# Kernel tuning notes

Measured on AMD Instinct MI355X. Metric: run time of the kernel, lower is better.

Reference implementation:

```python
import jax, jax.numpy as jnp
import numpy as np

BS, T, G, C = 64, 128, 36, 256
H = 256          # gaze LSTM hidden
P = 256          # spatial projected size
PT = 256         # temporal projected size
Q = 16           # queue size
NC = 10          # num classes
NEG = -1e9


def setup_inputs() -> dict:
    key = jax.random.key(0)
    ks = jax.random.split(key, 40)
    s = 0.02
    D = C + H
    inp = {
        'cnn_feat_seq': jax.random.normal(ks[0], (BS, T, G, C), jnp.float32),
        'gaze_seq': jax.random.normal(ks[1], (BS, T, 3), jnp.float32),
        # init-hidden / init-cell MLPs (Linear(3,H), Tanh, Linear(H,H), Tanh)
        'init_h_w1': jax.random.normal(ks[2], (H, 3)) * s, 'init_h_b1': jnp.zeros((H,)),
        'init_h_w2': jax.random.normal(ks[3], (H, H)) * s, 'init_h_b2': jnp.zeros((H,)),
        'init_c_w1': jax.random.normal(ks[4], (H, 3)) * s, 'init_c_b1': jnp.zeros((H,)),
        'init_c_w2': jax.random.normal(ks[5], (H, H)) * s, 'init_c_b2': jnp.zeros((H,)),
        # LSTM (input 3, hidden H), torch gate order i,f,g,o
        'lstm_wih': jax.random.normal(ks[6], (4 * H, 3)) * s, 'lstm_whh': jax.random.normal(ks[7], (4 * H, H)) * s,
        'lstm_bih': jnp.zeros((4 * H,)), 'lstm_bhh': jnp.zeros((4 * H,)),
        # spatial attention
        'sa_wl': jax.random.normal(ks[8], (P, H)) * s, 'sa_bl': jnp.zeros((P,)),
        'sa_wc': jax.random.normal(ks[9], (P, C)) * s, 'sa_bc': jnp.zeros((P,)),
        'sa_wz': jax.random.normal(ks[10], (P,)) * s,
        # temporal attention
        'ta_wl': jax.random.normal(ks[11], (PT, H)) * s, 'ta_bl': jnp.zeros((PT,)),
        'ta_wv': jax.random.normal(ks[12], (PT, C)) * s, 'ta_bv': jnp.zeros((PT,)),
        'ta_wz': jax.random.normal(ks[13], (PT,)) * s,
        # MLP classifier: Linear(D,D) -> Linear(D,D) -> Linear(D,NC), no nonlinearity
        'mlp_w1': jax.random.normal(ks[14], (D, D)) * s, 'mlp_b1': jnp.zeros((D,)),
        'mlp_w2': jax.random.normal(ks[15], (D, D)) * s, 'mlp_b2': jnp.zeros((D,)),
        'mlp_w3': jax.random.normal(ks[16], (NC, D)) * s, 'mlp_b3': jnp.zeros((NC,)),
    }
    return inp


def _forward(cnn_feat_seq, gaze_seq,
             init_h_w1, init_h_b1, init_h_w2, init_h_b2,
             init_c_w1, init_c_b1, init_c_w2, init_c_b2,
             lstm_wih, lstm_whh, lstm_bih, lstm_bhh,
             sa_wl, sa_bl, sa_wc, sa_bc, sa_wz,
             ta_wl, ta_bl, ta_wv, ta_bv, ta_wz,
             mlp_w1, mlp_b1, mlp_w2, mlp_b2, mlp_w3, mlp_b3):
    bs, num_frame = gaze_seq.shape[0], gaze_seq.shape[1]
    mean_gaze = jnp.mean(gaze_seq, axis=1)  # (bs, 3)
    # init MLP ends with Tanh, and forward applies F.tanh again
    h0 = jnp.tanh(jnp.tanh(jnp.tanh(mean_gaze @ init_h_w1.T + init_h_b1) @ init_h_w2.T + init_h_b2))
    c0 = jnp.tanh(jnp.tanh(jnp.tanh(mean_gaze @ init_c_w1.T + init_c_b1) @ init_c_w2.T + init_c_b2))
    buf_s0 = jnp.zeros((Q, bs, C), cnn_feat_seq.dtype)
    buf_h0 = jnp.zeros((Q, bs, H), cnn_feat_seq.dtype)
    qidx = jnp.arange(Q)

    def step(carry, xs):
        h, c, buf_s, buf_h, i = carry
        feat, gaze = xs  # (bs,G,C), (bs,3)
        # --- spatial additive attention over grids ---
        Hp = h @ sa_wl.T + sa_bl                                  # (bs,P)
        Vp = jnp.einsum('bgc,pc->bgp', feat, sa_wc) + sa_bc       # (bs,G,P)
        zs = jnp.tanh(Hp[:, None, :] + Vp) @ sa_wz                # (bs,G)
        sw = jax.nn.softmax(zs, axis=1)
        spat = jnp.einsum('bgc,bg->bc', feat, sw)                 # (bs,C)
        # --- rolling queues (newest last) ---
        buf_s = jnp.concatenate([buf_s[1:], spat[None]], axis=0)
        buf_h = jnp.concatenate([buf_h[1:], h[None]], axis=0)
        count = jnp.minimum(i + 1, Q)
        mask = qidx >= (Q - count)                                # (Q,) valid slots
        # --- temporal additive attention over queue ---
        Hq = jnp.einsum('qbh,ph->qbp', buf_h, ta_wl) + ta_bl
        Vq = jnp.einsum('qbc,pc->qbp', buf_s, ta_wv) + ta_bv
        zt = jnp.tanh(Hq + Vq) @ ta_wz                            # (Q,bs)
        zt = jnp.where(mask[:, None], zt, NEG)
        tw = jax.nn.softmax(zt, axis=0)
        temp = jnp.einsum('qbc,qb->bc', buf_s, tw)                # (bs,C)
        # --- one LSTM step on gaze ---
        gates = gaze @ lstm_wih.T + lstm_bih + h @ lstm_whh.T + lstm_bhh
        gi, gf, gg, go = jnp.split(gates, 4, axis=-1)
        c = jax.nn.sigmoid(gf) * c + jax.nn.sigmoid(gi) * jnp.tanh(gg)
        h = jax.nn.sigmoid(go) * jnp.tanh(c)
        # --- classifier on concat(temporal_feat, lstm_hidden) ---
        fc = jnp.concatenate([temp, h], axis=1)                   # (bs, C+H)
        pred = ((fc @ mlp_w1.T + mlp_b1) @ mlp_w2.T + mlp_b2) @ mlp_w3.T + mlp_b3
        return (h, c, buf_s, buf_h, i + 1), pred

    feats_t = jnp.swapaxes(cnn_feat_seq, 0, 1)  # (T,bs,G,C)
    gaze_t = jnp.swapaxes(gaze_seq, 0, 1)       # (T,bs,3)
    _, preds = jax.lax.scan(step, (h0, c0, buf_s0, buf_h0, jnp.int32(0)), (feats_t, gaze_t))
    # torch cats (1,bs,NC) pieces along dim=1 -> (1, T*bs, NC)
    return preds.reshape(1, num_frame * bs, NC)


def reference(cnn_feat_seq, gaze_seq,
              init_h_w1, init_h_b1, init_h_w2, init_h_b2,
              init_c_w1, init_c_b1, init_c_w2, init_c_b2,
              lstm_wih, lstm_whh, lstm_bih, lstm_bhh,
              sa_wl, sa_bl, sa_wc, sa_bc, sa_wz,
              ta_wl, ta_bl, ta_wv, ta_bv, ta_wz,
              mlp_w1, mlp_b1, mlp_w2, mlp_b2, mlp_w3, mlp_b3):
    return _forward(cnn_feat_seq, gaze_seq,
                    init_h_w1, init_h_b1, init_h_w2, init_h_b2,
                    init_c_w1, init_c_b1, init_c_w2, init_c_b2,
                    lstm_wih, lstm_whh, lstm_bih, lstm_bhh,
                    sa_wl, sa_bl, sa_wc, sa_bc, sa_wz,
                    ta_wl, ta_bl, ta_wv, ta_bv, ta_wz,
                    mlp_w1, mlp_b1, mlp_w2, mlp_b2, mlp_w3, mlp_b3)
```

## Files before the change

### kernel.cpp

```cpp
#include <hip/hip_runtime.h>
#include <cstdint>
#include <cstddef>

#define BSZ 64
#define TT  128
#define GG  36
#define CC  256
#define HH  256
#define QQ  16
#define NCLS 10
#define NROW 8192
#define SP_ROWS 16

using short8  = __attribute__((ext_vector_type(8))) short;
using f32x4   = __attribute__((ext_vector_type(4))) float;
using half2_t = __attribute__((ext_vector_type(2))) _Float16;
typedef unsigned int u32;
typedef unsigned short u16;

#define OFF_WI    0u
#define OFF_WF    131072u
#define OFF_WG    262144u
#define OFF_WO    393216u
#define OFF_SAWL  524288u
#define OFF_TAWL  655360u
#define OFF_TAWV  786432u
#define OFF_SAWC  917504u
#define OFF_W32   1048576u
#define OFF_WC    1069056u
#define OFF_BC    1089536u
#define OFF_H0F16 1089792u
#define OFF_C0    1122560u
#define OFF_HSEQ  1188096u
#define OFF_HSEQB 9642240u
#define OFF_HPSA  13869312u
#define OFF_HQ    22257920u
#define OFF_SPAT  30646528u
#define OFF_SPATB 39035136u
#define OFF_ZSC   43229440u
#define WS_NEEDED 43262208u

__device__ __forceinline__ float rcp_fast(float x){
#if __has_builtin(__builtin_amdgcn_rcpf)
  return __builtin_amdgcn_rcpf(x);
#else
  return 1.f/x;
#endif
}
__device__ __forceinline__ float fast_sig(float x){ return rcp_fast(1.f+__expf(-x)); }
__device__ __forceinline__ float fast_tanh(float x){ float e=__expf(2.f*x); return 1.f-2.f*rcp_fast(e+1.f); }
__device__ __forceinline__ u16 f2bf(float f){
  u32 u = __builtin_bit_cast(u32, f);
  u += 0x7fffu + ((u>>16)&1u);
  return (u16)(u>>16);
}
__device__ __forceinline__ float bf2f(u16 b){
  u32 u = ((u32)b)<<16; return __builtin_bit_cast(float, u);
}
__device__ __forceinline__ u32 cvtpk_bf16(float a, float b){
  u32 p;
  asm("v_cvt_pk_bf16_f32 %0, %1, %2" : "=v"(p) : "v"(a), "v"(b));
  return p;
}
__device__ __forceinline__ u32 packf16(float a, float b){
  half2_t h; h.x = (_Float16)a; h.y = (_Float16)b;
  return __builtin_bit_cast(u32, h);
}
__device__ __forceinline__ float dot2(u32 w, u32 h, float acc){
#if __has_builtin(__builtin_amdgcn_fdot2)
  return __builtin_amdgcn_fdot2(__builtin_bit_cast(half2_t, w),
                                __builtin_bit_cast(half2_t, h), acc, false);
#else
  half2_t a = __builtin_bit_cast(half2_t, w), b = __builtin_bit_cast(half2_t, h);
  return acc + (float)a.x*(float)b.x + (float)a.y*(float)b.y;
#endif
}
__device__ __forceinline__ f32x4 mfma16(short8 a, short8 b, f32x4 c){
  return __builtin_amdgcn_mfma_f32_16x16x32_bf16(a, b, c, 0, 0, 0);
}

__global__ void __launch_bounds__(256) k_prep1(const float* __restrict__ whh,
    const float* __restrict__ sawl, const float* __restrict__ tawl,
    const float* __restrict__ tawv, const float* __restrict__ sawc,
    const float* __restrict__ w3, const float* __restrict__ w2, char* ws){
  int blk = blockIdx.x, tid = threadIdx.x;
  if (blk < 512){
    u32* wq = (u32*)ws;
    for (int rr = 0; rr < 2; ++rr){
      int row = blk*2 + rr;
      float v  = whh[row*256 + tid];
      float vn = __shfl_down(v, 1);
      if ((tid & 1) == 0){
        int typ = row >> 8;
        int j   = row & 255;
        wq[typ*32768 + (tid>>1)*256 + j] = packf16(v, vn);
      }
    }
  } else if (blk < 544){
    int rel = blk - 512;
    int mat = rel >> 3;
    const float* src; u16* dst;
    if (mat==0){ src=sawl; dst=(u16*)(ws+OFF_SAWL); }
    else if (mat==1){ src=tawl; dst=(u16*)(ws+OFF_TAWL); }
    else if (mat==2){ src=tawv; dst=(u16*)(ws+OFF_TAWV); }
    else { src=sawc; dst=(u16*)(ws+OFF_SAWC); }
    int base = (rel & 7)*8192 + tid;
    if (mat < 3){
      for (int i = 0; i < 32; ++i){ int e = base + i*256; dst[e] = f2bf(src[e]); }
    } else {
      for (int i = 0; i < 32; ++i){
        int e = base + i*256;
        int col = e >> 8, kk = e & 255;
        dst[col*256 + (kk ^ ((col&7)<<3))] = f2bf(src[e]);
      }
    }
  } else {
    int idx = (blk-544)*256 + tid;
    int o = idx >> 9, k2 = idx & 511;
    float acc = 0.f;
    for (int m = 0; m < 512; ++m) acc = fmaf(w3[o*512+m], w2[m*512+k2], acc);
    ((float*)(ws+OFF_W32))[idx] = acc;
  }
}

__global__ void __launch_bounds__(256) k_prep2(const float* __restrict__ w1,
    const float* __restrict__ b1, const float* __restrict__ w3,
    const float* __restrict__ b2, const float* __restrict__ b3,
    const float* __restrict__ gaze,
    const float* __restrict__ ihw1, const float* __restrict__ ihb1,
    const float* __restrict__ ihw2, const float* __restrict__ ihb2,
    const float* __restrict__ icw1, const float* __restrict__ icb1,
    const float* __restrict__ icw2, const float* __restrict__ icb2,
    char* ws){
  int blk = blockIdx.x, tid = threadIdx.x;
  const float* W32 = (const float*)(ws+OFF_W32);
  if (blk < 20){
    int idx = blk*256 + tid; int o = idx>>9, k = idx&511;
    float acc = 0.f;
    for (int m = 0; m < 512; ++m) acc = fmaf(W32[o*512+m], w1[m*512+k], acc);
    ((float*)(ws+OFF_WC))[idx] = acc;
  } else if (blk == 20){
    if (tid < 10){
      float acc = b3[tid];
      for (int m = 0; m < 512; ++m) acc = fmaf(W32[tid*512+m], b1[m], acc);
      for (int m = 0; m < 512; ++m) acc = fmaf(w3[tid*512+m], b2[m], acc);
      ((float*)(ws+OFF_BC))[tid] = acc;
    }
  } else {
    int b = blk - 21;
    __shared__ float red0[128], red1[128], red2[128];
    __shared__ float mg[3];
    __shared__ float x1[256];
    if (tid < 128){
      const float* gp = gaze + b*384 + tid*3;
      red0[tid] = gp[0]; red1[tid] = gp[1]; red2[tid] = gp[2];
    }
    __syncthreads();
    for (int s = 64; s >= 1; s >>= 1){
      if (tid < s){ red0[tid]+=red0[tid+s]; red1[tid]+=red1[tid+s]; red2[tid]+=red2[tid+s]; }
      __syncthreads();
    }
    if (tid == 0){ mg[0]=red0[0]*(1.f/128.f); mg[1]=red1[0]*(1.f/128.f); mg[2]=red2[0]*(1.f/128.f); }
    __syncthreads();
    for (int which = 0; which < 2; ++which){
      const float* aw1 = which? icw1 : ihw1; const float* ab1 = which? icb1 : ihb1;
      const float* aw2 = which? icw2 : ihw2; const float* ab2 = which? icb2 : ihb2;
      float v = fast_tanh(fmaf(aw1[tid*3+2],mg[2], fmaf(aw1[tid*3+1],mg[1], fmaf(aw1[tid*3],mg[0], ab1[tid]))));
      x1[tid] = v;
      __syncthreads();
      float acc = ab2[tid];
      for (int k = 0; k < 256; ++k) acc = fmaf(aw2[tid*256+k], x1[k], acc);
      float h0 = fast_tanh(fast_tanh(acc));
      if (which == 0){
        float* hseq = (float*)(ws+OFF_HSEQ);
        hseq[(size_t)(0*64 + b)*256 + tid] = h0;
        float hn = __shfl_down(h0, 1);
        if ((tid&1)==0){
          ((u32*)(ws+OFF_HSEQB))[((size_t)(0*64+b)*256 + tid)>>1] = ((u32)f2bf(hn)<<16) | f2bf(h0);
          ((u32*)(ws+OFF_H0F16))[b*128 + (tid>>1)] = packf16(h0, hn);
        }
      } else {
        ((float*)(ws+OFF_C0))[b*256 + tid] = h0;
      }
      __syncthreads();
    }
  }
}

__global__ void __launch_bounds__(512, 2) k_lstm(const float* __restrict__ gaze,
    const float* __restrict__ wih, const float* __restrict__ bih,
    const float* __restrict__ bhh, char* ws){
  int b = blockIdx.x, tid = threadIdx.x;
  int half = tid >> 8;
  int j = tid & 255;
  __shared__ u32 lds_w[16*2048];
  __shared__ __align__(16) u32 hbuf[2][128];
  __shared__ float p_lds[256];
  __shared__ float g_lds[384];

  const u32* wq = (const u32*)ws;
  const u32* wA = wq + (half ? 1 : 0) * 32768;
  const u32* wB = wq + (half ? 3 : 2) * 32768;
  u32 w0[128], w1r[64];
#pragma unroll
  for (int c = 0; c < 128; ++c) w0[c] = wA[c*256 + j];
#pragma unroll
  for (int c = 0; c < 64; ++c)  w1r[c] = wB[c*256 + j];
#pragma unroll
  for (int cq = 0; cq < 16; ++cq)
#pragma unroll
    for (int q = 0; q < 4; ++q)
      lds_w[cq*2048 + tid*4 + q] = wB[(64 + cq*4 + q)*256 + j];

  if (tid < 384) g_lds[tid] = gaze[b*384 + tid];
  if (tid < 128) hbuf[0][tid] = ((const u32*)(ws+OFF_H0F16))[b*128 + tid];
  float creg = half ? ((const float*)(ws+OFF_C0))[b*256 + j] : 0.f;

  int rA = half ? 256 + j : j;
  int rB = half ? 768 + j : 512 + j;
  float baseA = bih[rA] + bhh[rA];
  float baseB = bih[rB] + bhh[rB];
  float uA0 = wih[rA*3], uA1 = wih[rA*3+1], uA2 = wih[rA*3+2];
  float uB0 = wih[rB*3], uB1 = wih[rB*3+1], uB2 = wih[rB*3+2];

  float* hseq = (float*)(ws+OFF_HSEQ);
  u32* hseqb = (u32*)(ws+OFF_HSEQB);
  float hv_prev = 0.f; u32 hpk_prev = 0;
  __syncthreads();

  for (int t = 0; t < 128; ++t){
    int cur = t & 1, nxt = cur ^ 1;
    if (half == 1 && t > 0){
      hseq[((size_t)t*64 + b)*256 + j] = hv_prev;
      if ((j & 1) == 0)
        hseqb[(((size_t)t*64 + b)*256 + j)>>1] = hpk_prev;
    }
    float g0 = g_lds[t*3], g1 = g_lds[t*3+1], g2 = g_lds[t*3+2];
    float aA0 = fmaf(uA2,g2, fmaf(uA1,g1, fmaf(uA0,g0, baseA))), aA1 = 0.f;
    float aB0 = fmaf(uB2,g2, fmaf(uB1,g1, fmaf(uB0,g0, baseB))), aB1 = 0.f;
#pragma unroll
    for (int c4 = 0; c4 < 32; ++c4){
      uint4 h4 = *reinterpret_cast<const uint4*>(&hbuf[cur][c4*4]);
      u32 wb0, wb1, wb2, wb3;
      if (c4 < 16){
        wb0 = w1r[c4*4]; wb1 = w1r[c4*4+1]; wb2 = w1r[c4*4+2]; wb3 = w1r[c4*4+3];
      } else {
        uint4 wv = *reinterpret_cast<const uint4*>(&lds_w[(c4-16)*2048 + tid*4]);
        wb0 = wv.x; wb1 = wv.y; wb2 = wv.z; wb3 = wv.w;
      }
      aA0 = dot2(w0[c4*4+0], h4.x, aA0); aB0 = dot2(wb0, h4.x, aB0);
      aA1 = dot2(w0[c4*4+1], h4.y, aA1); aB1 = dot2(wb1, h4.y, aB1);
      aA0 = dot2(w0[c4*4+2], h4.z, aA0); aB0 = dot2(wb2, h4.z, aB0);
      aA1 = dot2(w0[c4*4+3], h4.w, aA1); aB1 = dot2(wb3, h4.w, aB1);
    }
    float aA = aA0 + aA1, aB = aB0 + aB1;
    if (half == 0){
      p_lds[j] = fast_sig(aA) * fast_tanh(aB);
    }
    __syncthreads();
    if (half == 1){
      float p = p_lds[j];
      creg = fmaf(fast_sig(aA), creg, p);
      float hv = fast_sig(aB) * fast_tanh(creg);
      float hn = __shfl_down(hv, 1);
      if ((j & 1) == 0) hbuf[nxt][j>>1] = packf16(hv, hn);
      hv_prev = hv;
      hpk_prev = ((u32)f2bf(hn)<<16) | f2bf(hv);
    }
    __syncthreads();
  }
  if (half == 1){
    hseq[((size_t)128*64 + b)*256 + j] = hv_prev;
    if ((j & 1) == 0)
      hseqb[(((size_t)128*64 + b)*256 + j)>>1] = hpk_prev;
  }
}

__global__ void __launch_bounds__(256) k_proj1(const float* __restrict__ sabl,
    const float* __restrict__ sabc, const float* __restrict__ tabl,
    const float* __restrict__ tabv, char* ws){
  int bx = blockIdx.x, which = blockIdx.y;
  const u16* A = (const u16*)(ws+OFF_HSEQB);
  const u16* B = (const u16*)(ws + (which? OFF_TAWL : OFF_SAWL));
  float* Out   = (float*)(ws + (which? OFF_HQ : OFF_HPSA));
  const float* bp1 = which? tabl : sabl;
  const float* bp2 = which? tabv : sabc;
  int tid = threadIdx.x, w = tid>>6, l = tid&63;
  int lr = l&15, lk = l>>4;
  int rb = bx*64;
  short8 afr[4][8];
#pragma unroll
  for (int m = 0; m < 4; ++m)
#pragma unroll
    for (int k = 0; k < 8; ++k)
      afr[m][k] = *(const short8*)(const void*)(A + (size_t)(rb + m*16 + lr)*256 + k*32 + lk*8);
#pragma unroll
  for (int n = 0; n < 4; ++n){
    int cb = w*64 + n*16;
    int col = cb + lr;
    float bias = bp1[col] + bp2[col];
    f32x4 a0 = {0.f,0.f,0.f,0.f}, a1 = a0, a2 = a0, a3 = a0;
#pragma unroll
    for (int k = 0; k < 8; ++k){
      short8 bf = *(const short8*)(const void*)(B + (size_t)col*256 + k*32 + lk*8);
      a0 = mfma16(afr[0][k], bf, a0);
      a1 = mfma16(afr[1][k], bf, a1);
      a2 = mfma16(afr[2][k], bf, a2);
      a3 = mfma16(afr[3][k], bf, a3);
    }
#pragma unroll
    for (int q = 0; q < 4; ++q){
      Out[(size_t)(rb + 0*16 + lk*4 + q)*256 + col] = a0[q] + bias;
      Out[(size_t)(rb + 1*16 + lk*4 + q)*256 + col] = a1[q] + bias;
      Out[(size_t)(rb + 2*16 + lk*4 + q)*256 + col] = a2[q] + bias;
      Out[(size_t)(rb + 3*16 + lk*4 + q)*256 + col] = a3[q] + bias;
    }
  }
}

__global__ void __launch_bounds__(512, 2) k_spatial(const float* __restrict__ feat,
    const float* __restrict__ sawz, char* ws){
  __shared__ __align__(16) u16 featb[48*256];
  __shared__ __align__(16) float hp[256];
  __shared__ float wzs[256];
  __shared__ float zsbuf[8][48];
  __shared__ float swl[36];
  __shared__ float psum[2][256];
  int bx = blockIdx.x, tid = threadIdx.x, w = tid>>6, l = tid&63;
  int lr = l&15, lk = l>>4;
  int colbase = w*32;
  const float* hpsa = (const float*)(ws+OFF_HPSA);
  const u16* Bw = (const u16*)(ws+OFF_SAWC);

  short8 breg[2][8];
#pragma unroll
  for (int n = 0; n < 2; ++n){
    int col = colbase + n*16 + lr;
#pragma unroll
    for (int k = 0; k < 8; ++k)
      breg[n][k] = *(const short8*)(const void*)(Bw + (size_t)col*256 + ((k*32 + lk*8) ^ ((col&7)<<3)));
  }
  if (tid < 256) wzs[tid] = sawz[tid];

  float4 pf[5]; float4 ph;
  {
    int r0 = bx*SP_ROWS;
    int t = r0>>6, b = r0&63;
    const float4* fb = (const float4*)(feat + ((size_t)(b*128 + t))*9216);
#pragma unroll
    for (int ii = 0; ii < 4; ++ii) pf[ii] = fb[tid + ii*512];
    if (tid < 256) pf[4] = fb[2048 + tid];
    if (tid < 64) ph = ((const float4*)(hpsa + (size_t)r0*256))[tid];
  }
  __syncthreads();

  for (int i = 0; i < SP_ROWS; ++i){
    int r = bx*SP_ROWS + i;
#pragma unroll
    for (int ii = 0; ii < 4; ++ii){
      int e = tid + ii*512;
      int g = e >> 6, c4 = e & 63;
      uint2 pp;
      pp.x = cvtpk_bf16(pf[ii].x, pf[ii].y);
      pp.y = cvtpk_bf16(pf[ii].z, pf[ii].w);
      *reinterpret_cast<uint2*>((u32*)featb + g*128 + ((c4*2) ^ ((g&7)<<2))) = pp;
    }
    if (tid < 256){
      int e = 2048 + tid;
      int g = e >> 6, c4 = e & 63;
      uint2 pp;
      pp.x = cvtpk_bf16(pf[4].x, pf[4].y);
      pp.y = cvtpk_bf16(pf[4].z, pf[4].w);
      *reinterpret_cast<uint2*>((u32*)featb + g*128 + ((c4*2) ^ ((g&7)<<2))) = pp;
    }
    if (tid < 64) *reinterpret_cast<float4*>(hp + tid*4) = ph;
    __syncthreads();
    if (i + 1 < SP_ROWS){
      int rn = r + 1;
      int t = rn>>6, b = rn&63;
      const float4* fb = (const float4*)(feat + ((size_t)(b*128 + t))*9216);
#pragma unroll
      for (int ii = 0; ii < 4; ++ii) pf[ii] = fb[tid + ii*512];
      if (tid < 256) pf[4] = fb[2048 + tid];
      if (tid < 64) ph = ((const float4*)(hpsa + (size_t)rn*256))[tid];
    }
    float zacc[3][4] = {{0.f}};
#pragma unroll
    for (int m = 0; m < 3; ++m){
      short8 afr[8];
#pragma unroll
      for (int k = 0; k < 8; ++k){
        int g = m*16 + lr;
        afr[k] = *(const short8*)(const void*)(featb + g*256 + ((k*32 + lk*8) ^ ((g&7)<<3)));
      }
#pragma unroll
      for (int n = 0; n < 2; ++n){
        f32x4 a = {0.f,0.f,0.f,0.f};
#pragma unroll
        for (int k = 0; k < 8; ++k) a = mfma16(afr[k], breg[n][k], a);
        int col = colbase + n*16 + lr;
        float hpl = hp[col], wzv = wzs[col];
#pragma unroll
        for (int q = 0; q < 4; ++q)
          zacc[m][q] += fast_tanh(a[q] + hpl)*wzv;
      }
    }
#pragma unroll
    for (int m = 0; m < 3; ++m)
#pragma unroll
      for (int q = 0; q < 4; ++q){
        float v = zacc[m][q];
        v += __shfl_xor(v, 1); v += __shfl_xor(v, 2);
        v += __shfl_xor(v, 4); v += __shfl_xor(v, 8);
        if (lr == 0) zsbuf[w][m*16 + lk*4 + q] = v;
      }
    __syncthreads();
    if (w == 0){
      float z = -1e30f;
      if (l < 36)
        z = zsbuf[0][l]+zsbuf[1][l]+zsbuf[2][l]+zsbuf[3][l]
          + zsbuf[4][l]+zsbuf[5][l]+zsbuf[6][l]+zsbuf[7][l];
      float mx = z;
      for (int d = 1; d < 64; d <<= 1) mx = fmaxf(mx, __shfl_xor(mx, d));
      float e = (l < 36)? __expf(z - mx) : 0.f;
      float s = e;
      for (int d = 1; d < 64; d <<= 1) s += __shfl_xor(s, d);
      if (l < 36) swl[l] = e * rcp_fast(s);
    }
    __syncthreads();
    {
      int hsel = tid >> 8, col = tid & 255;
      float part = 0.f;
#pragma unroll
      for (int gg = 0; gg < 18; ++gg){
        int g = hsel*18 + gg;
        part = fmaf(swl[g], bf2f(featb[g*256 + (col ^ ((g&7)<<3))]), part);
      }
      psum[hsel][col] = part;
    }
    __syncthreads();
    if (tid < 256){
      float acc = psum[0][tid] + psum[1][tid];
      ((float*)(ws+OFF_SPAT))[(size_t)r*256 + tid] = acc;
      float an = __shfl_down(acc, 1);
      if ((tid & 1) == 0)
        ((u32*)(ws+OFF_SPATB))[((size_t)r*256 + tid)>>1] = cvtpk_bf16(acc, an);
    }
  }
}

__global__ void __launch_bounds__(256) k_proj2(const float* __restrict__ tawz, char* ws){
  int bx = blockIdx.x;
  int tid = threadIdx.x, w = tid>>6, l = tid&63;
  int lr = l&15, lk = l>>4;
  int rb = bx*64;
  const u16* A = (const u16*)(ws+OFF_SPATB);
  const u16* B = (const u16*)(ws+OFF_TAWV);
  const float* Hq = (const float*)(ws+OFF_HQ);
  __shared__ float zbuf[4][64];
  short8 afr[4][8];
#pragma unroll
  for (int m = 0; m < 4; ++m)
#pragma unroll
    for (int k = 0; k < 8; ++k)
      afr[m][k] = *(const short8*)(const void*)(A + (size_t)(rb + m*16 + lr)*256 + k*32 + lk*8);
  float racc[4][4] = {{0.f}};
#pragma unroll
  for (int n = 0; n < 4; ++n){
    int col = w*64 + n*16 + lr;
    float tzl = tawz[col];
    f32x4 a0 = {0.f,0.f,0.f,0.f}, a1 = a0, a2 = a0, a3 = a0;
#pragma unroll
    for (int k = 0; k < 8; ++k){
      short8 bf = *(const short8*)(const void*)(B + (size_t)col*256 + k*32 + lk*8);
      a0 = mfma16(afr[0][k], bf, a0);
      a1 = mfma16(afr[1][k], bf, a1);
      a2 = mfma16(afr[2][k], bf, a2);
      a3 = mfma16(afr[3][k], bf, a3);
    }
#pragma unroll
    for (int q = 0; q < 4; ++q){
      racc[0][q] += fast_tanh(a0[q] + Hq[(size_t)(rb + 0*16 + lk*4 + q)*256 + col]) * tzl;
      racc[1][q] += fast_tanh(a1[q] + Hq[(size_t)(rb + 1*16 + lk*4 + q)*256 + col]) * tzl;
      racc[2][q] += fast_tanh(a2[q] + Hq[(size_t)(rb + 2*16 + lk*4 + q)*256 + col]) * tzl;
      racc[3][q] += fast_tanh(a3[q] + Hq[(size_t)(rb + 3*16 + lk*4 + q)*256 + col]) * tzl;
    }
  }
#pragma unroll
  for (int m = 0; m < 4; ++m)
#pragma unroll
    for (int q = 0; q < 4; ++q){
      float v = racc[m][q];
      v += __shfl_xor(v, 1); v += __shfl_xor(v, 2);
      v += __shfl_xor(v, 4); v += __shfl_xor(v, 8);
      if (lr == 0) zbuf[w][m*16 + lk*4 + q] = v;
    }
  __syncthreads();
  if (tid < 64)
    ((float*)(ws+OFF_ZSC))[rb + tid] = zbuf[0][tid]+zbuf[1][tid]+zbuf[2][tid]+zbuf[3][tid];
}

__global__ void __launch_bounds__(256) k_final(float* __restrict__ out, char* ws){
  int bx = blockIdx.x;
  int b = bx & 63, tb = bx >> 6;
  int t0 = tb*8;
  int tid = threadIdx.x;
  int wv = tid>>6, l = tid&63;
  __shared__ float spw[23][256];
  __shared__ float zw[23];
  __shared__ float WcL[5120];
  __shared__ float bcL[10];
  __shared__ float w16[16];
  __shared__ float wpart[4][10];
  const float* spat = (const float*)(ws+OFF_SPAT);
  const float* zsc  = (const float*)(ws+OFF_ZSC);
  const float* hseq = (const float*)(ws+OFF_HSEQ);
  const float* Wc   = (const float*)(ws+OFF_WC);
#pragma unroll
  for (int i = 0; i < 20; ++i) WcL[tid + i*256] = Wc[tid + i*256];
  if (tid < 10) bcL[tid] = ((const float*)(ws+OFF_BC))[tid];
  for (int i = 0; i < 23; ++i){
    int tau = t0 - 15 + i;
    spw[i][tid] = (tau >= 0)? spat[(size_t)(tau*64 + b)*256 + tid] : 0.f;
  }
  if (tid < 23){
    int tau = t0 - 15 + tid;
    zw[tid] = (tau >= 0)? zsc[tau*64 + b] : -1e9f;
  }
  __syncthreads();
  for (int dt = 0; dt < 8; ++dt){
    int t = t0 + dt;
    if (wv == 0 && l < 16){
      float z = zw[dt + l];
      float mx = z;
      mx = fmaxf(mx, __shfl_xor(mx,1)); mx = fmaxf(mx, __shfl_xor(mx,2));
      mx = fmaxf(mx, __shfl_xor(mx,4)); mx = fmaxf(mx, __shfl_xor(mx,8));
      float e = __expf(z - mx);
      float s = e;
      s += __shfl_xor(s,1); s += __shfl_xor(s,2); s += __shfl_xor(s,4); s += __shfl_xor(s,8);
      w16[l] = e / s;
    }
    __syncthreads();
    float temp = 0.f;
#pragma unroll
    for (int qi = 0; qi < 16; ++qi) temp = fmaf(w16[qi], spw[dt+qi][tid], temp);
    float hc = hseq[(size_t)((t+1)*64 + b)*256 + tid];
    float po[10];
#pragma unroll
    for (int o = 0; o < 10; ++o){
      float v = fmaf(temp, WcL[o*512 + tid], hc*WcL[o*512 + 256 + tid]);
      v += __shfl_xor(v,1);  v += __shfl_xor(v,2);  v += __shfl_xor(v,4);
      v += __shfl_xor(v,8);  v += __shfl_xor(v,16); v += __shfl_xor(v,32);
      po[o] = v;
    }
    if (l == 0){
#pragma unroll
      for (int o = 0; o < 10; ++o) wpart[wv][o] = po[o];
    }
    __syncthreads();
    if (tid < 10)
      out[(size_t)(t*64 + b)*10 + tid] = wpart[0][tid]+wpart[1][tid]+wpart[2][tid]+wpart[3][tid] + bcL[tid];
    __syncthreads();
  }
}

extern "C" void kernel_launch(void* const* d_in, const int* in_sizes, int n_in,
                              void* d_out, int out_size, void* d_ws, size_t ws_size,
                              hipStream_t stream){
  const float* feat = (const float*)d_in[0];
  const float* gaze = (const float*)d_in[1];
  const float* ihw1 = (const float*)d_in[2];  const float* ihb1 = (const float*)d_in[3];
  const float* ihw2 = (const float*)d_in[4];  const float* ihb2 = (const float*)d_in[5];
  const float* icw1 = (const float*)d_in[6];  const float* icb1 = (const float*)d_in[7];
  const float* icw2 = (const float*)d_in[8];  const float* icb2 = (const float*)d_in[9];
  const float* wih  = (const float*)d_in[10]; const float* whh  = (const float*)d_in[11];
  const float* bih  = (const float*)d_in[12]; const float* bhh  = (const float*)d_in[13];
  const float* sawl = (const float*)d_in[14]; const float* sabl = (const float*)d_in[15];
  const float* sawc = (const float*)d_in[16]; const float* sabc = (const float*)d_in[17];
  const float* sawz = (const float*)d_in[18];
  const float* tawl = (const float*)d_in[19]; const float* tabl = (const float*)d_in[20];
  const float* tawv = (const float*)d_in[21]; const float* tabv = (const float*)d_in[22];
  const float* tawz = (const float*)d_in[23];
  const float* w1 = (const float*)d_in[24]; const float* b1 = (const float*)d_in[25];
  const float* w2 = (const float*)d_in[26]; const float* b2 = (const float*)d_in[27];
  const float* w3 = (const float*)d_in[28]; const float* b3 = (const float*)d_in[29];
  char* ws = (char*)d_ws;
  float* out = (float*)d_out;
  if (ws_size < (size_t)WS_NEEDED) return;

  k_prep1<<<dim3(564), dim3(256), 0, stream>>>(whh, sawl, tawl, tawv, sawc, w3, w2, ws);
  k_prep2<<<dim3(85), dim3(256), 0, stream>>>(w1, b1, w3, b2, b3, gaze,
      ihw1, ihb1, ihw2, ihb2, icw1, icb1, icw2, icb2, ws);
  k_lstm<<<dim3(64), dim3(512), 0, stream>>>(gaze, wih, bih, bhh, ws);
  k_proj1<<<dim3(128, 2), dim3(256), 0, stream>>>(sabl, sabc, tabl, tabv, ws);
  k_spatial<<<dim3(512), dim3(512), 0, stream>>>(feat, sawz, ws);
  k_proj2<<<dim3(128), dim3(256), 0, stream>>>(tawz, ws);
  k_final<<<dim3(1024), dim3(256), 0, stream>>>(out, ws);
}
```

Baseline: 491.0 us.

## Convert features to bf16 in idle blocks alongside serial LSTM kernel

Result: slower. 503.0 us (+2.4%).

```diff
diff --git a/kernel.cpp b/kernel.cpp
--- a/kernel.cpp
+++ b/kernel.cpp
@@ -39,6 +39,8 @@
 #define OFF_SPATB 39035136u
 #define OFF_ZSC   43229440u
 #define WS_NEEDED 43262208u
+#define OFF_FEATB 43262208u
+#define WS_NEED_BIG 194257152u
 
 __device__ __forceinline__ float rcp_fast(float x){
 #if __has_builtin(__builtin_amdgcn_rcpf)
@@ -187,6 +189,127 @@
   }
 }
 
+__global__ void __launch_bounds__(512, 2) k_lstm_vp(const float* __restrict__ gaze,
+    const float* __restrict__ wih, const float* __restrict__ bih,
+    const float* __restrict__ bhh, const float* __restrict__ feat, char* ws){
+  __shared__ u32 lds_w[16*2048];
+  __shared__ __align__(16) u32 hbuf[2][128];
+  __shared__ float p_lds[256];
+  __shared__ float g_lds[384];
+  int tid = threadIdx.x;
+
+  if (blockIdx.x >= 64){
+    int cb = blockIdx.x - 64;
+    u32* fbg = (u32*)(ws + OFF_FEATB);
+    for (int r = cb; r < NROW; r += 192){
+      int t = r >> 6, b = r & 63;
+      const float4* fb = (const float4*)(feat + ((size_t)(b*128 + t))*9216);
+      u32* dst = fbg + (size_t)r*4608;
+#pragma unroll
+      for (int ii = 0; ii < 4; ++ii){
+        int e = tid + ii*512;
+        float4 v = fb[e];
+        int g = e >> 6, c4 = e & 63;
+        uint2 pp;
+        pp.x = cvtpk_bf16(v.x, v.y);
+        pp.y = cvtpk_bf16(v.z, v.w);
+        *reinterpret_cast<uint2*>(dst + g*128 + ((c4*2) ^ ((g&7)<<2))) = pp;
+      }
+      if (tid < 256){
+        int e = 2048 + tid;
+        float4 v = fb[e];
+        int g = e >> 6, c4 = e & 63;
+        uint2 pp;
+        pp.x = cvtpk_bf16(v.x, v.y);
+        pp.y = cvtpk_bf16(v.z, v.w);
+        *reinterpret_cast<uint2*>(dst + g*128 + ((c4*2) ^ ((g&7)<<2))) = pp;
+      }
+    }
+    return;
+  }
+
+  int b = blockIdx.x;
+  int half = tid >> 8;
+  int j = tid & 255;
+
+  const u32* wq = (const u32*)ws;
+  const u32* wA = wq + (half ? 1 : 0) * 32768;
+  const u32* wB = wq + (half ? 3 : 2) * 32768;
+  u32 w0[128], w1r[64];
+#pragma unroll
+  for (int c = 0; c < 128; ++c) w0[c] = wA[c*256 + j];
+#pragma unroll
+  for (int c = 0; c < 64; ++c)  w1r[c] = wB[c*256 + j];
+#pragma unroll
+  for (int cq = 0; cq < 16; ++cq)
+#pragma unroll
+    for (int q = 0; q < 4; ++q)
+      lds_w[cq*2048 + tid*4 + q] = wB[(64 + cq*4 + q)*256 + j];
+
+  if (tid < 384) g_lds[tid] = gaze[b*384 + tid];
+  if (tid < 128) hbuf[0][tid] = ((const u32*)(ws+OFF_H0F16))[b*128 + tid];
+  float creg = half ? ((const float*)(ws+OFF_C0))[b*256 + j] : 0.f;
+
+  int rA = half ? 256 + j : j;
+  int rB = half ? 768 + j : 512 + j;
+  float baseA = bih[rA] + bhh[rA];
+  float baseB = bih[rB] + bhh[rB];
+  float uA0 = wih[rA*3], uA1 = wih[rA*3+1], uA2 = wih[rA*3+2];
+  float uB0 = wih[rB*3], uB1 = wih[rB*3+1], uB2 = wih[rB*3+2];
+
+  float* hseq = (float*)(ws+OFF_HSEQ);
+  u32* hseqb = (u32*)(ws+OFF_HSEQB);
+  float hv_prev = 0.f; u32 hpk_prev = 0;
+  __syncthreads();
+
+  for (int t = 0; t < 128; ++t){
+    int cur = t & 1, nxt = cur ^ 1;
+    if (half == 1 && t > 0){
+      hseq[((size_t)t*64 + b)*256 + j] = hv_prev;
+      if ((j & 1) == 0)
+        hseqb[(((size_t)t*64 + b)*256 + j)>>1] = hpk_prev;
+    }
+    float g0 = g_lds[t*3], g1 = g_lds[t*3+1], g2 = g_lds[t*3+2];
+    float aA0 = fmaf(uA2,g2, fmaf(uA1,g1, fmaf(uA0,g0, baseA))), aA1 = 0.f;
+    float aB0 = fmaf(uB2,g2, fmaf(uB1,g1, fmaf(uB0,g0, baseB))), aB1 = 0.f;
+#pragma unroll
+    for (int c4 = 0; c4 < 32; ++c4){
+      uint4 h4 = *reinterpret_cast<const uint4*>(&hbuf[cur][c4*4]);
+      u32 wb0, wb1, wb2, wb3;
+      if (c4 < 16){
+        wb0 = w1r[c4*4]; wb1 = w1r[c4*4+1]; wb2 = w1r[c4*4+2]; wb3 = w1r[c4*4+3];
+      } else {
+        uint4 wv = *reinterpret_cast<const uint4*>(&lds_w[(c4-16)*2048 + tid*4]);
+        wb0 = wv.x; wb1 = wv.y; wb2 = wv.z; wb3 = wv.w;
+      }
+      aA0 = dot2(w0[c4*4+0], h4.x, aA0); aB0 = dot2(wb0, h4.x, aB0);
+      aA1 = dot2(w0[c4*4+1], h4.y, aA1); aB1 = dot2(wb1, h4.y, aB1);
+      aA0 = dot2(w0[c4*4+2], h4.z, aA0); aB0 = dot2(wb2, h4.z, aB0);
+      aA1 = dot2(w0[c4*4+3], h4.w, aA1); aB1 = dot2(wb3, h4.w, aB1);
+    }
+    float aA = aA0 + aA1, aB = aB0 + aB1;
+    if (half == 0){
+      p_lds[j] = fast_sig(aA) * fast_tanh(aB);
+    }
+    __syncthreads();
+    if (half == 1){
+      float p = p_lds[j];
+      creg = fmaf(fast_sig(aA), creg, p);
+      float hv = fast_sig(aB) * fast_tanh(creg);
+      float hn = __shfl_down(hv, 1);
+      if ((j & 1) == 0) hbuf[nxt][j>>1] = packf16(hv, hn);
+      hv_prev = hv;
+      hpk_prev = ((u32)f2bf(hn)<<16) | f2bf(hv);
+    }
+    __syncthreads();
+  }
+  if (half == 1){
+    hseq[((size_t)128*64 + b)*256 + j] = hv_prev;
+    if ((j & 1) == 0)
+      hseqb[(((size_t)128*64 + b)*256 + j)>>1] = hpk_prev;
+  }
+}
+
 __global__ void __launch_bounds__(512, 2) k_lstm(const float* __restrict__ gaze,
     const float* __restrict__ wih, const float* __restrict__ bih,
     const float* __restrict__ bhh, char* ws){
@@ -314,6 +437,125 @@
       Out[(size_t)(rb + 1*16 + lk*4 + q)*256 + col] = a1[q] + bias;
       Out[(size_t)(rb + 2*16 + lk*4 + q)*256 + col] = a2[q] + bias;
       Out[(size_t)(rb + 3*16 + lk*4 + q)*256 + col] = a3[q] + bias;
+    }
+  }
+}
+
+__global__ void __launch_bounds__(512, 2) k_spatial_fin(const float* __restrict__ sawz,
+    char* ws){
+  __shared__ __align__(16) u16 featb[48*256];
+  __shared__ __align__(16) float hp[256];
+  __shared__ float wzs[256];
+  __shared__ float zsbuf[8][48];
+  __shared__ float swl[36];
+  __shared__ float psum[2][256];
+  int bx = blockIdx.x, tid = threadIdx.x, w = tid>>6, l = tid&63;
+  int lr = l&15, lk = l>>4;
+  int colbase = w*32;
+  const float* hpsa = (const float*)(ws+OFF_HPSA);
+  const u16* Bw = (const u16*)(ws+OFF_SAWC);
+  const uint2* fbg = (const uint2*)(ws + OFF_FEATB);
+
+  short8 breg[2][8];
+#pragma unroll
+  for (int n = 0; n < 2; ++n){
+    int col = colbase + n*16 + lr;
+#pragma unroll
+    for (int k = 0; k < 8; ++k)
+      breg[n][k] = *(const short8*)(const void*)(Bw + (size_t)col*256 + ((k*32 + lk*8) ^ ((col&7)<<3)));
+  }
+  if (tid < 256) wzs[tid] = sawz[tid];
+
+  uint2 pf2[5]; float4 ph;
+  {
+    int r0 = bx*SP_ROWS;
+    const uint2* src = fbg + (size_t)r0*2304;
+#pragma unroll
+    for (int ii = 0; ii < 4; ++ii) pf2[ii] = src[tid + ii*512];
+    if (tid < 256) pf2[4] = src[2048 + tid];
+    if (tid < 64) ph = ((const float4*)(hpsa + (size_t)r0*256))[tid];
+  }
+  __syncthreads();
+
+  for (int i = 0; i < SP_ROWS; ++i){
+    int r = bx*SP_ROWS + i;
+    {
+      uint2* lds2 = (uint2*)featb;
+#pragma unroll
+      for (int ii = 0; ii < 4; ++ii) lds2[tid + ii*512] = pf2[ii];
+      if (tid < 256) lds2[2048 + tid] = pf2[4];
+      if (tid < 64) *reinterpret_cast<float4*>(hp + tid*4) = ph;
+    }
+    __syncthreads();
+    if (i + 1 < SP_ROWS){
+      int rn = r + 1;
+      const uint2* src = fbg + (size_t)rn*2304;
+#pragma unroll
+      for (int ii = 0; ii < 4; ++ii) pf2[ii] = src[tid + ii*512];
+      if (tid < 256) pf2[4] = src[2048 + tid];
+      if (tid < 64) ph = ((const float4*)(hpsa + (size_t)rn*256))[tid];
+    }
+    float zacc[3][4] = {{0.f}};
+#pragma unroll
+    for (int m = 0; m < 3; ++m){
+      short8 afr[8];
+#pragma unroll
+      for (int k = 0; k < 8; ++k){
+        int g = m*16 + lr;
+        afr[k] = *(const short8*)(const void*)(featb + g*256 + ((k*32 + lk*8) ^ ((g&7)<<3)));
+      }
+#pragma unroll
+      for (int n = 0; n < 2; ++n){
+        f32x4 a = {0.f,0.f,0.f,0.f};
+#pragma unroll
+        for (int k = 0; k < 8; ++k) a = mfma16(afr[k], breg[n][k], a);
+        int col = colbase + n*16 + lr;
+        float hpl = hp[col], wzv = wzs[col];
+#pragma unroll
+        for (int q = 0; q < 4; ++q)
+          zacc[m][q] += fast_tanh(a[q] + hpl)*wzv;
+      }
+    }
+#pragma unroll
+    for (int m = 0; m < 3; ++m)
+#pragma unroll
+      for (int q = 0; q < 4; ++q){
+        float v = zacc[m][q];
+        v += __shfl_xor(v, 1); v += __shfl_xor(v, 2);
+        v += __shfl_xor(v, 4); v += __shfl_xor(v, 8);
+        if (lr == 0) zsbuf[w][m*16 + lk*4 + q] = v;
+      }
+    __syncthreads();
+    if (w == 0){
+      float z = -1e30f;
+      if (l < 36)
+        z = zsbuf[0][l]+zsbuf[1][l]+zsbuf[2][l]+zsbuf[3][l]
+          + zsbuf[4][l]+zsbuf[5][l]+zsbuf[6][l]+zsbuf[7][l];
+      float mx = z;
+      for (int d = 1; d < 64; d <<= 1) mx = fmaxf(mx, __shfl_xor(mx, d));
+      float e = (l < 36)? __expf(z - mx) : 0.f;
+      float s = e;
+      for (int d = 1; d < 64; d <<= 1) s += __shfl_xor(s, d);
+      if (l < 36) swl[l] = e * rcp_fast(s);
+    }
+    __syncthreads();
+    {
+      int hsel = tid >> 8, col = tid & 255;
+      float part = 0.f;
+#pragma unroll
+      for (int gg = 0; gg < 18; ++gg){
+        int g = hsel*18 + gg;
+        part = fmaf(swl[g], bf2f(featb[g*256 + (col ^ ((g&7)<<3))]), part);
+      }
+      psum[hsel][col] = part;
+    }
+    __syncthreads();
+    if (tid < 256){
+      float acc = psum[0][tid] + psum[1][tid];
+      ((float*)(ws+OFF_SPAT))[(size_t)r*256 + tid] = acc;
+      float an = __shfl_down(acc, 1);
+      if ((tid & 1) == 0)
+        ((u32*)(ws+OFF_SPATB))[((size_t)r*256 + tid)>>1] = cvtpk_bf16(acc, an);
     }
   }
 }
@@ -587,13 +829,20 @@
   char* ws = (char*)d_ws;
   float* out = (float*)d_out;
   if (ws_size < (size_t)WS_NEEDED) return;
+  bool big = ws_size >= (size_t)WS_NEED_BIG;
 
   k_prep1<<<dim3(564), dim3(256), 0, stream>>>(whh, sawl, tawl, tawv, sawc, w3, w2, ws);
   k_prep2<<<dim3(85), dim3(256), 0, stream>>>(w1, b1, w3, b2, b3, gaze,
       ihw1, ihb1, ihw2, ihb2, icw1, icb1, icw2, icb2, ws);
-  k_lstm<<<dim3(64), dim3(512), 0, stream>>>(gaze, wih, bih, bhh, ws);
-  k_proj1<<<dim3(128, 2), dim3(256), 0, stream>>>(sabl, sabc, tabl, tabv, ws);
-  k_spatial<<<dim3(512), dim3(512), 0, stream>>>(feat, sawz, ws);
+  if (big){
+    k_lstm_vp<<<dim3(256), dim3(512), 0, stream>>>(gaze, wih, bih, bhh, feat, ws);
+    k_proj1<<<dim3(128, 2), dim3(256), 0, stream>>>(sabl, sabc, tabl, tabv, ws);
+    k_spatial_fin<<<dim3(512), dim3(512), 0, stream>>>(sawz, ws);
+  } else {
+    k_lstm<<<dim3(64), dim3(512), 0, stream>>>(gaze, wih, bih, bhh, ws);
+    k_proj1<<<dim3(128, 2), dim3(256), 0, stream>>>(sabl, sabc, tabl, tabv, ws);
+    k_spatial<<<dim3(512), dim3(512), 0, stream>>>(feat, sawz, ws);
+  }
   k_proj2<<<dim3(128), dim3(256), 0, stream>>>(tawz, ws);
   k_final<<<dim3(1024), dim3(256), 0, stream>>>(out, ws);
 }
```
